# Kernel tuning notes

Measured on AMD Instinct MI355X. Metric: run time of the kernel, lower is better.

## Reference

```python
import math
import jax, jax.numpy as jnp
import numpy as np

B, S, D, H = 64, 577, 768, 12
DH = D // H          # 64 per-head dim
FF = 4 * D           # 3072 intermediate
EPS = 1e-6


def layernorm(x, g, b):
    mu = jnp.mean(x, axis=-1, keepdims=True)
    var = jnp.mean(jnp.square(x - mu), axis=-1, keepdims=True)
    return (x - mu) * jax.lax.rsqrt(var + EPS) * g + b


def gelu_tanh(x):
    # NewGELUActivation: 0.5*x*(1+tanh(sqrt(2/pi)*(x+0.044715*x^3)))
    c = math.sqrt(2.0 / math.pi)
    return 0.5 * x * (1.0 + jnp.tanh(c * (x + 0.044715 * x ** 3)))


def setup_inputs() -> dict:
    key = jax.random.key(0)
    ks = jax.random.split(key, 16)
    s_d = 1.0 / math.sqrt(D)
    s_ff = 1.0 / math.sqrt(FF)
    return {
        "x": jax.random.normal(ks[0], (B, S, D), jnp.float32),
        "ln1_g": jnp.ones((D,), jnp.float32),
        "ln1_b": jnp.zeros((D,), jnp.float32),
        # per-head Q/K/V weights stacked: [H, D, DH] (equivalent to H separate Linears)
        "Wq": jax.random.normal(ks[1], (H, D, DH), jnp.float32) * s_d,
        "bq": jax.random.normal(ks[2], (H, DH), jnp.float32) * 0.01,
        "Wk": jax.random.normal(ks[3], (H, D, DH), jnp.float32) * s_d,
        "bk": jax.random.normal(ks[4], (H, DH), jnp.float32) * 0.01,
        "Wv": jax.random.normal(ks[5], (H, D, DH), jnp.float32) * s_d,
        "bv": jax.random.normal(ks[6], (H, DH), jnp.float32) * 0.01,
        "Wo": jax.random.normal(ks[7], (D, D), jnp.float32) * s_d,
        "bo": jax.random.normal(ks[8], (D,), jnp.float32) * 0.01,
        "ln2_g": jnp.ones((D,), jnp.float32),
        "ln2_b": jnp.zeros((D,), jnp.float32),
        "W1": jax.random.normal(ks[9], (D, FF), jnp.float32) * s_d,
        "b1": jax.random.normal(ks[10], (FF,), jnp.float32) * 0.01,
        "W2": jax.random.normal(ks[11], (FF, D), jnp.float32) * s_ff,
        "b2": jax.random.normal(ks[12], (D,), jnp.float32) * 0.01,
    }


def reference(x, ln1_g, ln1_b, Wq, bq, Wk, bk, Wv, bv, Wo, bo,
              ln2_g, ln2_b, W1, b1, W2, b2):
    # --- pre-norm MHA ---
    h = layernorm(x, ln1_g, ln1_b)                       # [B,S,D]
    q = jnp.einsum('bsd,hde->bhse', h, Wq) + bq[:, None, :]
    k = jnp.einsum('bsd,hde->bhse', h, Wk) + bk[:, None, :]
    v = jnp.einsum('bsd,hde->bhse', h, Wv) + bv[:, None, :]
    scores = jnp.einsum('bhse,bhte->bhst', q, k) / math.sqrt(DH)
    probs = jax.nn.softmax(scores, axis=-1)              # [B,H,S,S]
    attn = jnp.einsum('bhst,bhte->bhse', probs, v)       # [B,H,S,DH]
    # concat heads in head order -> [B,S,H*DH]
    concat = attn.transpose(0, 2, 1, 3).reshape(B, S, H * DH)
    x = x + concat @ Wo + bo
    # --- pre-norm MLP ---
    m = layernorm(x, ln2_g, ln2_b)
    m = gelu_tanh(m @ W1 + b1) @ W2 + b2
    return x + m
```

## Files before the change

### kernel.cpp

```cpp
#include <hip/hip_runtime.h>
#include <stdint.h>

constexpr int BZ   = 64;
constexpr int SEQ  = 577;
constexpr int DM   = 768;
constexpr int NH   = 12;
constexpr int HD   = 64;
constexpr int FFD  = 3072;
constexpr int ROWS = BZ * SEQ;
constexpr int BHN  = BZ * NH;
constexpr int VTS  = 640;

typedef __attribute__((ext_vector_type(8))) short bf16x8;
typedef __attribute__((ext_vector_type(4))) float f32x4;

static __device__ __forceinline__ unsigned short f2bf(float f) {
  union { float f; uint32_t u; } v; v.f = f;
  uint32_t r = (v.u + 0x7FFFu + ((v.u >> 16) & 1u)) >> 16;
  return (unsigned short)r;
}

static __device__ __forceinline__ f32x4 mfma16(bf16x8 a, bf16x8 b, f32x4 c) {
  return __builtin_amdgcn_mfma_f32_16x16x32_bf16(a, b, c, 0, 0, 0);
}

static __device__ __forceinline__ void gload_lds16(const unsigned short* g, unsigned short* l) {
  __builtin_amdgcn_global_load_lds((const __attribute__((address_space(1))) unsigned int*)g,
                                   (__attribute__((address_space(3))) unsigned int*)l, 16, 0, 0);
}

__global__ __launch_bounds__(256) void prep_qkv(const float* __restrict__ Wq,
                                                const float* __restrict__ Wk,
                                                const float* __restrict__ Wv,
                                                unsigned short* __restrict__ dst) {
  int tid = blockIdx.x * 256 + threadIdx.x;
  int n = tid / DM, k = tid - n * DM;
  int seg = n / DM;
  int within = n - seg * DM;
  int h = within >> 6, e = within & 63;
  const float* W = (seg == 0) ? Wq : (seg == 1) ? Wk : Wv;
  dst[tid] = f2bf(W[((size_t)h * DM + k) * HD + e]);
}

__global__ __launch_bounds__(256) void prep_t(const float* __restrict__ src,
                                              unsigned short* __restrict__ dst,
                                              int N, int K) {
  int tid = blockIdx.x * 256 + threadIdx.x;
  if (tid >= N * K) return;
  int n = tid / K, k = tid - n * K;
  dst[tid] = f2bf(src[(size_t)k * N + n]);
}

__global__ __launch_bounds__(256) void ln_bf16(const float* __restrict__ X,
                                               const float* __restrict__ g,
                                               const float* __restrict__ b,
                                               unsigned short* __restrict__ out) {
  int row  = blockIdx.x * 4 + (threadIdx.x >> 6);
  int lane = threadIdx.x & 63;
  const float* x = X + (size_t)row * DM;
  float4 v[3];
  float s = 0.f, s2 = 0.f;
#pragma unroll
  for (int i = 0; i < 3; i++) {
    v[i] = *(const float4*)(x + i * 256 + lane * 4);
    s  += v[i].x + v[i].y + v[i].z + v[i].w;
    s2 += v[i].x * v[i].x + v[i].y * v[i].y + v[i].z * v[i].z + v[i].w * v[i].w;
  }
#pragma unroll
  for (int o = 1; o < 64; o <<= 1) { s += __shfl_xor(s, o); s2 += __shfl_xor(s2, o); }
  float mu  = s * (1.f / DM);
  float var = s2 * (1.f / DM) - mu * mu;
  float inv = rsqrtf(var + 1e-6f);
#pragma unroll
  for (int i = 0; i < 3; i++) {
    int c = i * 256 + lane * 4;
    float4 gg = *(const float4*)(g + c);
    float4 bb = *(const float4*)(b + c);
    ushort4 o4;
    o4.x = f2bf((v[i].x - mu) * inv * gg.x + bb.x);
    o4.y = f2bf((v[i].y - mu) * inv * gg.y + bb.y);
    o4.z = f2bf((v[i].z - mu) * inv * gg.z + bb.z);
    o4.w = f2bf((v[i].w - mu) * inv * gg.w + bb.w);
    *(ushort4*)(out + (size_t)row * DM + c) = o4;
  }
}

template <int EPI>
__global__ __launch_bounds__(256) void gemm_bt(
    const unsigned short* __restrict__ A, const unsigned short* __restrict__ Bt,
    int M, int N, int K, int nbn,
    const float* __restrict__ bias0, const float* __restrict__ bias1,
    const float* __restrict__ bias2, const float* __restrict__ xres,
    float* __restrict__ outf,
    unsigned short* __restrict__ ob0, unsigned short* __restrict__ ob1,
    unsigned short* __restrict__ ob2) {
  __shared__ __align__(16) unsigned short sA[128 * 64];
  __shared__ __align__(16) unsigned short sB[128 * 64];
  const int tid  = threadIdx.x;
  const int wave = tid >> 6;
  const int lane = tid & 63;
  const int l15 = lane & 15, quad = lane >> 4;

  const int nb = gridDim.x;
  const int L = blockIdx.x;
  const int per = nb >> 3, rem = nb & 7;
  const int x8 = L & 7, i8 = L >> 3;
  const int g = x8 * per + (x8 < rem ? x8 : rem) + i8;
  const int mt = g / nbn, nt = g - mt * nbn;
  const int m0 = mt * 128, n0 = nt * 128;
  const int wm = (wave >> 1) * 64, wn = (wave & 1) * 64;

  const unsigned short* srcA[4];
  const unsigned short* srcB[4];
  int sOff[4];
#pragma unroll
  for (int j = 0; j < 4; j++) {
    int c = tid + j * 256;
    int row = c >> 3, col = c & 7;
    int kc = col ^ (row & 7);
    int ra = m0 + row; if (ra >= M) ra = M - 1;
    srcA[j] = A + (size_t)ra * K + kc * 8;
    srcB[j] = Bt + (size_t)(n0 + row) * K + kc * 8;
    sOff[j] = c * 8;
  }

  f32x4 acc[4][4] = {};
  const int nkt = K >> 6;
  for (int kt = 0; kt < nkt; ++kt) {
#pragma unroll
    for (int j = 0; j < 4; j++) {
      gload_lds16(srcA[j], sA + sOff[j]);
      gload_lds16(srcB[j], sB + sOff[j]);
    }
#pragma unroll
    for (int j = 0; j < 4; j++) { srcA[j] += 64; srcB[j] += 64; }
    __syncthreads();
#pragma unroll
    for (int h = 0; h < 2; h++) {
      bf16x8 aF[4], bF[4];
      const int swz = ((h << 2) | quad) ^ (l15 & 7);
#pragma unroll
      for (int mi = 0; mi < 4; mi++) aF[mi] = *(const bf16x8*)(sA + (wm + mi * 16 + l15) * 64 + swz * 8);
#pragma unroll
      for (int ni = 0; ni < 4; ni++) bF[ni] = *(const bf16x8*)(sB + (wn + ni * 16 + l15) * 64 + swz * 8);
#pragma unroll
      for (int mi = 0; mi < 4; mi++)
#pragma unroll
        for (int ni = 0; ni < 4; ni++) acc[mi][ni] = mfma16(aF[mi], bF[ni], acc[mi][ni]);
    }
    __syncthreads();
  }

  const int bb0  = m0 / SEQ;
  const int bb0s = bb0 * SEQ;
#pragma unroll
  for (int mi = 0; mi < 4; mi++) {
#pragma unroll
    for (int r = 0; r < 4; r++) {
      int mg = m0 + wm + mi * 16 + quad * 4 + r;
      if (mg >= M) continue;
      if constexpr (EPI == 0) {
        int ss = mg - bb0s, bb = bb0;
        if (ss >= SEQ) { ss -= SEQ; bb++; }
        int seg = n0 / DM;
        int within0 = n0 - seg * DM + wn;
#pragma unroll
        for (int ni = 0; ni < 4; ni++) {
          int wcol = within0 + ni * 16 + l15;
          int h = wcol >> 6, e = wcol & 63;
          float val = acc[mi][ni][r];
          if (seg == 0) {
            float qv = (val + bias0[wcol]) * 0.125f;
            ob0[((size_t)(bb * NH + h) * SEQ + ss) * HD + e] = f2bf(qv);
          } else if (seg == 1) {
            float kv = val + bias1[wcol];
            ob1[((size_t)(bb * NH + h) * SEQ + ss) * HD + e] = f2bf(kv);
          } else {
            float vv = val + bias2[wcol];
            ob2[((size_t)(bb * NH + h) * HD + e) * VTS + ss] = f2bf(vv);
          }
        }
      } else if constexpr (EPI == 1) {
        size_t base = (size_t)mg * DM;
#pragma unroll
        for (int ni = 0; ni < 4; ni++) {
          int col = n0 + wn + ni * 16 + l15;
          outf[base + col] = xres[base + col] + acc[mi][ni][r] + bias0[col];
        }
      } else if constexpr (EPI == 2) {
        size_t base = (size_t)mg * FFD;
#pragma unroll
        for (int ni = 0; ni < 4; ni++) {
          int col = n0 + wn + ni * 16 + l15;
          float xv = acc[mi][ni][r] + bias0[col];
          float x2 = xv * xv;
          float tp = fmaf(x2, 0.0713548163f, 1.5957691216f);
          float m2u = xv * tp;
          float e  = exp2f(m2u * -1.4426950408889634f);
          float gel = xv * __builtin_amdgcn_rcpf(1.f + e);
          ob0[base + col] = f2bf(gel);
        }
      } else {
        size_t base = (size_t)mg * DM;
#pragma unroll
        for (int ni = 0; ni < 4; ni++) {
          int col = n0 + wn + ni * 16 + l15;
          outf[base + col] += acc[mi][ni][r] + bias0[col];
        }
      }
    }
  }
}

__global__ __launch_bounds__(256) void attn_fused(
    const unsigned short* __restrict__ Q, const unsigned short* __restrict__ Kb,
    const unsigned short* __restrict__ Vt, unsigned short* __restrict__ Cc) {
  __shared__ __align__(16) unsigned short sK[64 * 72];
  __shared__ __align__(16) unsigned short sV[64 * 72];
  __shared__ __align__(16) unsigned short sP[4][16 * 72];
  const int tid  = threadIdx.x;
  const int wave = tid >> 6, lane = tid & 63;
  const int quad = lane >> 4, l15 = lane & 15;

  const int nb = gridDim.x;
  const int L = blockIdx.x;
  const int per = nb >> 3, rem = nb & 7;
  const int x8 = L & 7, i8 = L >> 3;
  const int g = x8 * per + (x8 < rem ? x8 : rem) + i8;
  const int bh = g / 10;
  const int q0 = (g - bh * 10) * 64;

  int qr = q0 + wave * 16 + l15; if (qr > SEQ - 1) qr = SEQ - 1;
  const unsigned short* qrow = Q + ((size_t)bh * SEQ + qr) * HD;
  bf16x8 aQ0 = *(const bf16x8*)(qrow + quad * 8);
  bf16x8 aQ1 = *(const bf16x8*)(qrow + 32 + quad * 8);

  constexpr float L2E = 1.4426950408889634f;
  constexpr float OFF = 10.f * L2E;

  float l[4] = {0.f, 0.f, 0.f, 0.f};
  f32x4 accO[4] = {};

  for (int t0 = 0; t0 < SEQ; t0 += 64) {
#pragma unroll
    for (int i = 0; i < 2; i++) {
      int c = tid + i * 256;
      int row = c >> 3, col = (c & 7) << 3;
      int tk = t0 + row; if (tk > SEQ - 1) tk = SEQ - 1;
      bf16x8 vk = *(const bf16x8*)(Kb + ((size_t)bh * SEQ + tk) * HD + col);
      bf16x8 vv = *(const bf16x8*)(Vt + ((size_t)bh * HD + row) * VTS + t0 + col);
      *(bf16x8*)(sK + row * 72 + col) = vk;
      *(bf16x8*)(sV + row * 72 + col) = vv;
    }
    __syncthreads();

    f32x4 s4[4];
#pragma unroll
    for (int ni = 0; ni < 4; ni++) {
      bf16x8 b0 = *(const bf16x8*)(sK + (ni * 16 + l15) * 72 + quad * 8);
      bf16x8 b1 = *(const bf16x8*)(sK + (ni * 16 + l15) * 72 + 32 + quad * 8);
      f32x4 a = {0.f, 0.f, 0.f, 0.f};
      a = mfma16(aQ0, b0, a);
      a = mfma16(aQ1, b1, a);
      s4[ni] = a;
    }
#pragma unroll
    for (int ni = 0; ni < 4; ni++) {
      if (t0 + ni * 16 + l15 >= SEQ) {
#pragma unroll
        for (int r = 0; r < 4; r++) s4[ni][r] = -3e38f;
      }
    }
#pragma unroll
    for (int r = 0; r < 4; r++) {
      float p0 = exp2f(fmaf(s4[0][r], L2E, -OFF));
      float p1 = exp2f(fmaf(s4[1][r], L2E, -OFF));
      float p2 = exp2f(fmaf(s4[2][r], L2E, -OFF));
      float p3 = exp2f(fmaf(s4[3][r], L2E, -OFF));
      l[r] += (p0 + p1) + (p2 + p3);
      uint32_t pk01, pk23;
      asm("v_cvt_pk_bf16_f32 %0, %1, %2" : "=v"(pk01) : "v"(p0), "v"(p1));
      asm("v_cvt_pk_bf16_f32 %0, %1, %2" : "=v"(pk23) : "v"(p2), "v"(p3));
      unsigned short* prow = sP[wave] + (quad * 4 + r) * 72 + l15;
      prow[0]  = (unsigned short)pk01;
      prow[16] = (unsigned short)(pk01 >> 16);
      prow[32] = (unsigned short)pk23;
      prow[48] = (unsigned short)(pk23 >> 16);
    }
    bf16x8 aP0 = *(const bf16x8*)(sP[wave] + l15 * 72 + quad * 8);
    bf16x8 aP1 = *(const bf16x8*)(sP[wave] + l15 * 72 + 32 + quad * 8);
#pragma unroll
    for (int ni = 0; ni < 4; ni++) {
      bf16x8 v0 = *(const bf16x8*)(sV + (ni * 16 + l15) * 72 + quad * 8);
      bf16x8 v1 = *(const bf16x8*)(sV + (ni * 16 + l15) * 72 + 32 + quad * 8);
      accO[ni] = mfma16(aP0, v0, accO[ni]);
      accO[ni] = mfma16(aP1, v1, accO[ni]);
    }
    __syncthreads();
  }

#pragma unroll
  for (int r = 0; r < 4; r++) {
#pragma unroll
    for (int o = 1; o < 16; o <<= 1) l[r] += __shfl_xor(l[r], o);
  }
  int bb = bh / NH, h = bh - bb * NH;
#pragma unroll
  for (int r = 0; r < 4; r++) {
    int ss = q0 + wave * 16 + quad * 4 + r;
    if (ss < SEQ) {
      float inv = __builtin_amdgcn_rcpf(l[r]);
      size_t base = ((size_t)bb * SEQ + ss) * DM + h * HD;
#pragma unroll
      for (int ni = 0; ni < 4; ni++)
        Cc[base + ni * 16 + l15] = f2bf(accO[ni][r] * inv);
    }
  }
}

extern "C" void kernel_launch(void* const* d_in, const int* in_sizes, int n_in,
                              void* d_out, int out_size, void* d_ws, size_t ws_size,
                              hipStream_t stream) {
  (void)in_sizes; (void)n_in; (void)out_size; (void)ws_size;
  const float* x     = (const float*)d_in[0];
  const float* ln1_g = (const float*)d_in[1];
  const float* ln1_b = (const float*)d_in[2];
  const float* Wq    = (const float*)d_in[3];
  const float* bq    = (const float*)d_in[4];
  const float* Wk    = (const float*)d_in[5];
  const float* bk    = (const float*)d_in[6];
  const float* Wv    = (const float*)d_in[7];
  const float* bv    = (const float*)d_in[8];
  const float* Wo    = (const float*)d_in[9];
  const float* bo    = (const float*)d_in[10];
  const float* ln2_g = (const float*)d_in[11];
  const float* ln2_b = (const float*)d_in[12];
  const float* W1    = (const float*)d_in[13];
  const float* b1    = (const float*)d_in[14];
  const float* W2    = (const float*)d_in[15];
  const float* b2    = (const float*)d_in[16];
  float* out = (float*)d_out;

  char* ws = (char*)d_ws;
  size_t off = 0;
  auto alloc = [&](size_t bytes) -> unsigned short* {
    unsigned short* p = (unsigned short*)(ws + off);
    off += (bytes + 255) & ~(size_t)255;
    return p;
  };
  unsigned short* h_bf  = alloc((size_t)ROWS * DM * 2);
  unsigned short* q_bf  = alloc((size_t)BHN * SEQ * HD * 2);
  unsigned short* k_bf  = alloc((size_t)BHN * SEQ * HD * 2);
  unsigned short* vt_bf = alloc((size_t)BHN * HD * VTS * 2);
  unsigned short* cc_bf = alloc((size_t)ROWS * DM * 2);
  unsigned short* g_bf = q_bf;
  unsigned short* wqkv_t = alloc((size_t)2304 * 768 * 2);
  unsigned short* w1_t   = alloc((size_t)3072 * 768 * 2);
  unsigned short* w2_t   = alloc((size_t)768 * 3072 * 2);
  unsigned short* wo_t   = alloc((size_t)768 * 768 * 2);

  prep_qkv<<<(2304 * 768) / 256, 256, 0, stream>>>(Wq, Wk, Wv, wqkv_t);
  prep_t<<<(3072 * 768) / 256, 256, 0, stream>>>(W1, w1_t, 3072, 768);
  prep_t<<<(768 * 3072) / 256, 256, 0, stream>>>(W2, w2_t, 768, 3072);
  prep_t<<<(768 * 768) / 256, 256, 0, stream>>>(Wo, wo_t, 768, 768);

  const int MB = (ROWS + 127) / 128;

  ln_bf16<<<ROWS / 4, 256, 0, stream>>>(x, ln1_g, ln1_b, h_bf);
  gemm_bt<0><<<MB * 18, 256, 0, stream>>>(
      h_bf, wqkv_t, ROWS, 2304, 768, 18, bq, bk, bv, nullptr, nullptr, q_bf, k_bf, vt_bf);
  attn_fused<<<10 * BHN, 256, 0, stream>>>(q_bf, k_bf, vt_bf, cc_bf);
  gemm_bt<1><<<MB * 6, 256, 0, stream>>>(
      cc_bf, wo_t, ROWS, 768, 768, 6, bo, nullptr, nullptr, x, out, nullptr, nullptr, nullptr);
  ln_bf16<<<ROWS / 4, 256, 0, stream>>>(out, ln2_g, ln2_b, h_bf);
  gemm_bt<2><<<MB * 24, 256, 0, stream>>>(
      h_bf, w1_t, ROWS, 3072, 768, 24, b1, nullptr, nullptr, nullptr, nullptr, g_bf, nullptr, nullptr);
  gemm_bt<3><<<MB * 6, 256, 0, stream>>>(
      g_bf, w2_t, ROWS, 768, 3072, 6, b2, nullptr, nullptr, nullptr, out, nullptr, nullptr, nullptr);
}
```

Before: 1.355 ms.

## Double query rows per attention block and stage GELU output via LDS

The attention kernel now handles 128 query rows per block (two 64-row sub-tiles per wave) instead of 64. Each staged K/V tile is therefore reused twice, halving global K/V traffic and the block count. Separately, the FFN1 GELU epilogue writes its bf16 results into a swizzled LDS tile and then stores 16-byte coalesced rows, replacing scattered 2-byte global stores, with a scalar fallback for partial tiles. This adds register pressure in attention (double accumulators) and an extra barrier in the GEMM epilogue, and the final query block is now padded up to 640 rows.

```diff
diff --git a/kernel.cpp b/kernel.cpp
--- a/kernel.cpp
+++ b/kernel.cpp
@@ -94,8 +94,7 @@
     float* __restrict__ outf,
     unsigned short* __restrict__ ob0, unsigned short* __restrict__ ob1,
     unsigned short* __restrict__ ob2) {
-  __shared__ __align__(16) unsigned short sA[128 * 64];
-  __shared__ __align__(16) unsigned short sB[128 * 64];
+  __shared__ __align__(16) unsigned short sAB[2][128 * 64];
   const int tid  = threadIdx.x;
   const int wave = tid >> 6;
   const int lane = tid & 63;
@@ -129,8 +128,8 @@
   for (int kt = 0; kt < nkt; ++kt) {
 #pragma unroll
     for (int j = 0; j < 4; j++) {
-      gload_lds16(srcA[j], sA + sOff[j]);
-      gload_lds16(srcB[j], sB + sOff[j]);
+      gload_lds16(srcA[j], &sAB[0][sOff[j]]);
+      gload_lds16(srcB[j], &sAB[1][sOff[j]]);
     }
 #pragma unroll
     for (int j = 0; j < 4; j++) { srcA[j] += 64; srcB[j] += 64; }
@@ -140,9 +139,9 @@
       bf16x8 aF[4], bF[4];
       const int swz = ((h << 2) | quad) ^ (l15 & 7);
 #pragma unroll
-      for (int mi = 0; mi < 4; mi++) aF[mi] = *(const bf16x8*)(sA + (wm + mi * 16 + l15) * 64 + swz * 8);
-#pragma unroll
-      for (int ni = 0; ni < 4; ni++) bF[ni] = *(const bf16x8*)(sB + (wn + ni * 16 + l15) * 64 + swz * 8);
+      for (int mi = 0; mi < 4; mi++) aF[mi] = *(const bf16x8*)(&sAB[0][0] + (wm + mi * 16 + l15) * 64 + swz * 8);
+#pragma unroll
+      for (int ni = 0; ni < 4; ni++) bF[ni] = *(const bf16x8*)(&sAB[1][0] + (wn + ni * 16 + l15) * 64 + swz * 8);
 #pragma unroll
       for (int mi = 0; mi < 4; mi++)
 #pragma unroll
@@ -153,59 +152,100 @@
 
   const int bb0  = m0 / SEQ;
   const int bb0s = bb0 * SEQ;
-#pragma unroll
-  for (int mi = 0; mi < 4; mi++) {
-#pragma unroll
-    for (int r = 0; r < 4; r++) {
-      int mg = m0 + wm + mi * 16 + quad * 4 + r;
-      if (mg >= M) continue;
-      if constexpr (EPI == 0) {
-        int ss = mg - bb0s, bb = bb0;
-        if (ss >= SEQ) { ss -= SEQ; bb++; }
-        int seg = n0 / DM;
-        int within0 = n0 - seg * DM + wn;
-#pragma unroll
-        for (int ni = 0; ni < 4; ni++) {
-          int wcol = within0 + ni * 16 + l15;
-          int h = wcol >> 6, e = wcol & 63;
-          float val = acc[mi][ni][r];
-          if (seg == 0) {
-            float qv = (val + bias0[wcol]) * 0.125f;
-            ob0[((size_t)(bb * NH + h) * SEQ + ss) * HD + e] = f2bf(qv);
-          } else if (seg == 1) {
-            float kv = val + bias1[wcol];
-            ob1[((size_t)(bb * NH + h) * SEQ + ss) * HD + e] = f2bf(kv);
-          } else {
-            float vv = val + bias2[wcol];
-            ob2[((size_t)(bb * NH + h) * HD + e) * VTS + ss] = f2bf(vv);
+
+  if constexpr (EPI == 2) {
+    if (m0 + 128 <= M) {
+      unsigned short* sT = &sAB[0][0];
+#pragma unroll
+      for (int mi = 0; mi < 4; mi++) {
+#pragma unroll
+        for (int r = 0; r < 4; r++) {
+          int row = wm + mi * 16 + quad * 4 + r;
+#pragma unroll
+          for (int ni = 0; ni < 4; ni++) {
+            int col = wn + ni * 16 + l15;
+            float xv = acc[mi][ni][r] + bias0[n0 + col];
+            float x2 = xv * xv;
+            float tp = fmaf(x2, 0.0713548163f, 1.5957691216f);
+            float m2u = xv * tp;
+            float e  = exp2f(m2u * -1.4426950408889634f);
+            float gel = xv * __builtin_amdgcn_rcpf(1.f + e);
+            sT[row * 128 + (col ^ ((row & 7) << 4))] = f2bf(gel);
           }
         }
-      } else if constexpr (EPI == 1) {
-        size_t base = (size_t)mg * DM;
-#pragma unroll
-        for (int ni = 0; ni < 4; ni++) {
-          int col = n0 + wn + ni * 16 + l15;
-          outf[base + col] = xres[base + col] + acc[mi][ni][r] + bias0[col];
+      }
+      __syncthreads();
+#pragma unroll
+      for (int k = 0; k < 8; k++) {
+        int cid = tid + k * 256;
+        int row = cid >> 4, c16 = cid & 15;
+        bf16x8 v = *(const bf16x8*)(sT + row * 128 + ((c16 * 8) ^ ((row & 7) << 4)));
+        *(bf16x8*)(ob0 + (size_t)(m0 + row) * FFD + n0 + c16 * 8) = v;
+      }
+    } else {
+#pragma unroll
+      for (int mi = 0; mi < 4; mi++) {
+#pragma unroll
+        for (int r = 0; r < 4; r++) {
+          int mg = m0 + wm + mi * 16 + quad * 4 + r;
+          if (mg >= M) continue;
+          size_t base = (size_t)mg * FFD;
+#pragma unroll
+          for (int ni = 0; ni < 4; ni++) {
+            int col = n0 + wn + ni * 16 + l15;
+            float xv = acc[mi][ni][r] + bias0[col];
+            float x2 = xv * xv;
+            float tp = fmaf(x2, 0.0713548163f, 1.5957691216f);
+            float m2u = xv * tp;
+            float e  = exp2f(m2u * -1.4426950408889634f);
+            float gel = xv * __builtin_amdgcn_rcpf(1.f + e);
+            ob0[base + col] = f2bf(gel);
+          }
         }
-      } else if constexpr (EPI == 2) {
-        size_t base = (size_t)mg * FFD;
-#pragma unroll
-        for (int ni = 0; ni < 4; ni++) {
-          int col = n0 + wn + ni * 16 + l15;
-          float xv = acc[mi][ni][r] + bias0[col];
-          float x2 = xv * xv;
-          float tp = fmaf(x2, 0.0713548163f, 1.5957691216f);
-          float m2u = xv * tp;
-          float e  = exp2f(m2u * -1.4426950408889634f);
-          float gel = xv * __builtin_amdgcn_rcpf(1.f + e);
-          ob0[base + col] = f2bf(gel);
-        }
-      } else {
-        size_t base = (size_t)mg * DM;
-#pragma unroll
-        for (int ni = 0; ni < 4; ni++) {
-          int col = n0 + wn + ni * 16 + l15;
-          outf[base + col] += acc[mi][ni][r] + bias0[col];
+      }
+    }
+  } else {
+#pragma unroll
+    for (int mi = 0; mi < 4; mi++) {
+#pragma unroll
+      for (int r = 0; r < 4; r++) {
+        int mg = m0 + wm + mi * 16 + quad * 4 + r;
+        if (mg >= M) continue;
+        if constexpr (EPI == 0) {
+          int ss = mg - bb0s, bb = bb0;
+          if (ss >= SEQ) { ss -= SEQ; bb++; }
+          int seg = n0 / DM;
+          int within0 = n0 - seg * DM + wn;
+#pragma unroll
+          for (int ni = 0; ni < 4; ni++) {
+            int wcol = within0 + ni * 16 + l15;
+            int h = wcol >> 6, e = wcol & 63;
+            float val = acc[mi][ni][r];
+            if (seg == 0) {
+              float qv = (val + bias0[wcol]) * 0.125f;
+              ob0[((size_t)(bb * NH + h) * SEQ + ss) * HD + e] = f2bf(qv);
+            } else if (seg == 1) {
+              float kv = val + bias1[wcol];
+              ob1[((size_t)(bb * NH + h) * SEQ + ss) * HD + e] = f2bf(kv);
+            } else {
+              float vv = val + bias2[wcol];
+              ob2[((size_t)(bb * NH + h) * HD + e) * VTS + ss] = f2bf(vv);
+            }
+          }
+        } else if constexpr (EPI == 1) {
+          size_t base = (size_t)mg * DM;
+#pragma unroll
+          for (int ni = 0; ni < 4; ni++) {
+            int col = n0 + wn + ni * 16 + l15;
+            outf[base + col] = xres[base + col] + acc[mi][ni][r] + bias0[col];
+          }
+        } else {
+          size_t base = (size_t)mg * DM;
+#pragma unroll
+          for (int ni = 0; ni < 4; ni++) {
+            int col = n0 + wn + ni * 16 + l15;
+            outf[base + col] += acc[mi][ni][r] + bias0[col];
+          }
         }
       }
     }
@@ -227,19 +267,24 @@
   const int per = nb >> 3, rem = nb & 7;
   const int x8 = L & 7, i8 = L >> 3;
   const int g = x8 * per + (x8 < rem ? x8 : rem) + i8;
-  const int bh = g / 10;
-  const int q0 = (g - bh * 10) * 64;
-
-  int qr = q0 + wave * 16 + l15; if (qr > SEQ - 1) qr = SEQ - 1;
-  const unsigned short* qrow = Q + ((size_t)bh * SEQ + qr) * HD;
-  bf16x8 aQ0 = *(const bf16x8*)(qrow + quad * 8);
-  bf16x8 aQ1 = *(const bf16x8*)(qrow + 32 + quad * 8);
+  const int bh = g / 5;
+  const int qb = (g - bh * 5) * 128;
+
+  int qr0 = qb + wave * 16 + l15; if (qr0 > SEQ - 1) qr0 = SEQ - 1;
+  int qr1 = qr0 + 64; if (qr1 > SEQ - 1) qr1 = SEQ - 1;
+  const unsigned short* q0p = Q + ((size_t)bh * SEQ + qr0) * HD;
+  const unsigned short* q1p = Q + ((size_t)bh * SEQ + qr1) * HD;
+  bf16x8 aQ[2][2];
+  aQ[0][0] = *(const bf16x8*)(q0p + quad * 8);
+  aQ[0][1] = *(const bf16x8*)(q0p + 32 + quad * 8);
+  aQ[1][0] = *(const bf16x8*)(q1p + quad * 8);
+  aQ[1][1] = *(const bf16x8*)(q1p + 32 + quad * 8);
 
   constexpr float L2E = 1.4426950408889634f;
   constexpr float OFF = 10.f * L2E;
 
-  float l[4] = {0.f, 0.f, 0.f, 0.f};
-  f32x4 accO[4] = {};
+  float l2[2][4] = {};
+  f32x4 accO[2][4] = {};
 
   for (int t0 = 0; t0 < SEQ; t0 += 64) {
 #pragma unroll
@@ -254,66 +299,74 @@
     }
     __syncthreads();
 
-    f32x4 s4[4];
-#pragma unroll
-    for (int ni = 0; ni < 4; ni++) {
-      bf16x8 b0 = *(const bf16x8*)(sK + (ni * 16 + l15) * 72 + quad * 8);
-      bf16x8 b1 = *(const bf16x8*)(sK + (ni * 16 + l15) * 72 + 32 + quad * 8);
-      f32x4 a = {0.f, 0.f, 0.f, 0.f};
-      a = mfma16(aQ0, b0, a);
-      a = mfma16(aQ1, b1, a);
-      s4[ni] = a;
-    }
-#pragma unroll
-    for (int ni = 0; ni < 4; ni++) {
-      if (t0 + ni * 16 + l15 >= SEQ) {
-#pragma unroll
-        for (int r = 0; r < 4; r++) s4[ni][r] = -3e38f;
-      }
-    }
+#pragma unroll
+    for (int u = 0; u < 2; u++) {
+      f32x4 s4[4];
+#pragma unroll
+      for (int ni = 0; ni < 4; ni++) {
+        bf16x8 b0 = *(const bf16x8*)(sK + (ni * 16 + l15) * 72 + quad * 8);
+        bf16x8 b1 = *(const bf16x8*)(sK + (ni * 16 + l15) * 72 + 32 + quad * 8);
+        f32x4 a = {0.f, 0.f, 0.f, 0.f};
+        a = mfma16(aQ[u][0], b0, a);
+        a = mfma16(aQ[u][1], b1, a);
+        s4[ni] = a;
+      }
+#pragma unroll
+      for (int ni = 0; ni < 4; ni++) {
+        if (t0 + ni * 16 + l15 >= SEQ) {
+#pragma unroll
+          for (int r = 0; r < 4; r++) s4[ni][r] = -3e38f;
+        }
+      }
+#pragma unroll
+      for (int r = 0; r < 4; r++) {
+        float p0 = exp2f(fmaf(s4[0][r], L2E, -OFF));
+        float p1 = exp2f(fmaf(s4[1][r], L2E, -OFF));
+        float p2 = exp2f(fmaf(s4[2][r], L2E, -OFF));
+        float p3 = exp2f(fmaf(s4[3][r], L2E, -OFF));
+        l2[u][r] += (p0 + p1) + (p2 + p3);
+        uint32_t pk01, pk23;
+        asm("v_cvt_pk_bf16_f32 %0, %1, %2" : "=v"(pk01) : "v"(p0), "v"(p1));
+        asm("v_cvt_pk_bf16_f32 %0, %1, %2" : "=v"(pk23) : "v"(p2), "v"(p3));
+        unsigned short* prow = sP[wave] + (quad * 4 + r) * 72 + l15;
+        prow[0]  = (unsigned short)pk01;
+        prow[16] = (unsigned short)(pk01 >> 16);
+        prow[32] = (unsigned short)pk23;
+        prow[48] = (unsigned short)(pk23 >> 16);
+      }
+      bf16x8 aP0 = *(const bf16x8*)(sP[wave] + l15 * 72 + quad * 8);
+      bf16x8 aP1 = *(const bf16x8*)(sP[wave] + l15 * 72 + 32 + quad * 8);
+#pragma unroll
+      for (int ni = 0; ni < 4; ni++) {
+        bf16x8 v0 = *(const bf16x8*)(sV + (ni * 16 + l15) * 72 + quad * 8);
+        bf16x8 v1 = *(const bf16x8*)(sV + (ni * 16 + l15) * 72 + 32 + quad * 8);
+        accO[u][ni] = mfma16(aP0, v0, accO[u][ni]);
+        accO[u][ni] = mfma16(aP1, v1, accO[u][ni]);
+      }
+    }
+    __syncthreads();
+  }
+
+#pragma unroll
+  for (int u = 0; u < 2; u++)
 #pragma unroll
     for (int r = 0; r < 4; r++) {
-      float p0 = exp2f(fmaf(s4[0][r], L2E, -OFF));
-      float p1 = exp2f(fmaf(s4[1][r], L2E, -OFF));
-      float p2 = exp2f(fmaf(s4[2][r], L2E, -OFF));
-      float p3 = exp2f(fmaf(s4[3][r], L2E, -OFF));
-      l[r] += (p0 + p1) + (p2 + p3);
-      uint32_t pk01, pk23;
-      asm("v_cvt_pk_bf16_f32 %0, %1, %2" : "=v"(pk01) : "v"(p0), "v"(p1));
-      asm("v_cvt_pk_bf16_f32 %0, %1, %2" : "=v"(pk23) : "v"(p2), "v"(p3));
-      unsigned short* prow = sP[wave] + (quad * 4 + r) * 72 + l15;
-      prow[0]  = (unsigned short)pk01;
-      prow[16] = (unsigned short)(pk01 >> 16);
-      prow[32] = (unsigned short)pk23;
-      prow[48] = (unsigned short)(pk23 >> 16);
-    }
-    bf16x8 aP0 = *(const bf16x8*)(sP[wave] + l15 * 72 + quad * 8);
-    bf16x8 aP1 = *(const bf16x8*)(sP[wave] + l15 * 72 + 32 + quad * 8);
-#pragma unroll
-    for (int ni = 0; ni < 4; ni++) {
-      bf16x8 v0 = *(const bf16x8*)(sV + (ni * 16 + l15) * 72 + quad * 8);
-      bf16x8 v1 = *(const bf16x8*)(sV + (ni * 16 + l15) * 72 + 32 + quad * 8);
-      accO[ni] = mfma16(aP0, v0, accO[ni]);
-      accO[ni] = mfma16(aP1, v1, accO[ni]);
-    }
-    __syncthreads();
-  }
-
-#pragma unroll
-  for (int r = 0; r < 4; r++) {
-#pragma unroll
-    for (int o = 1; o < 16; o <<= 1) l[r] += __shfl_xor(l[r], o);
-  }
+#pragma unroll
+      for (int o = 1; o < 16; o <<= 1) l2[u][r] += __shfl_xor(l2[u][r], o);
+    }
   int bb = bh / NH, h = bh - bb * NH;
 #pragma unroll
-  for (int r = 0; r < 4; r++) {
-    int ss = q0 + wave * 16 + quad * 4 + r;
-    if (ss < SEQ) {
-      float inv = __builtin_amdgcn_rcpf(l[r]);
-      size_t base = ((size_t)bb * SEQ + ss) * DM + h * HD;
-#pragma unroll
-      for (int ni = 0; ni < 4; ni++)
-        Cc[base + ni * 16 + l15] = f2bf(accO[ni][r] * inv);
+  for (int u = 0; u < 2; u++) {
+#pragma unroll
+    for (int r = 0; r < 4; r++) {
+      int ss = qb + u * 64 + wave * 16 + quad * 4 + r;
+      if (ss < SEQ) {
+        float inv = __builtin_amdgcn_rcpf(l2[u][r]);
+        size_t base = ((size_t)bb * SEQ + ss) * DM + h * HD;
+#pragma unroll
+        for (int ni = 0; ni < 4; ni++)
+          Cc[base + ni * 16 + l15] = f2bf(accO[u][ni][r] * inv);
+      }
     }
   }
 }
@@ -369,7 +422,7 @@
   ln_bf16<<<ROWS / 4, 256, 0, stream>>>(x, ln1_g, ln1_b, h_bf);
   gemm_bt<0><<<MB * 18, 256, 0, stream>>>(
       h_bf, wqkv_t, ROWS, 2304, 768, 18, bq, bk, bv, nullptr, nullptr, q_bf, k_bf, vt_bf);
-  attn_fused<<<10 * BHN, 256, 0, stream>>>(q_bf, k_bf, vt_bf, cc_bf);
+  attn_fused<<<5 * BHN, 256, 0, stream>>>(q_bf, k_bf, vt_bf, cc_bf);
   gemm_bt<1><<<MB * 6, 256, 0, stream>>>(
       cc_bf, wo_t, ROWS, 768, 768, 6, bo, nullptr, nullptr, x, out, nullptr, nullptr, nullptr);
   ln_bf16<<<ROWS / 4, 256, 0, stream>>>(out, ln2_g, ln2_b, h_bf);
```

Result: slower. 1.454 ms (+7.3%).
